# Optimization experiments

Hardware: AMD Instinct MI355X
Metric: run time of the kernel (lower is better)

The kernel has to match this reference:

```python
import jax, jax.numpy as jnp
import numpy as np

N_NODES = 100000
N_EDGES = 3200000
IN_CH = 256
HIDDEN = 64
OUT_CH = 128


def setup_inputs() -> dict:
    key = jax.random.key(0)
    ks = jax.random.split(key, 6)
    x = jax.random.normal(ks[0], (N_NODES, IN_CH), dtype=jnp.float32)
    edge_index = jax.random.randint(ks[1], (2, N_EDGES), 0, N_NODES, dtype=jnp.int64)
    W1 = jax.random.normal(ks[2], (IN_CH, HIDDEN), dtype=jnp.float32) * (1.0 / np.sqrt(IN_CH))
    b1 = jnp.zeros((HIDDEN,), dtype=jnp.float32)
    W2 = jax.random.normal(ks[3], (HIDDEN, OUT_CH), dtype=jnp.float32) * (1.0 / np.sqrt(HIDDEN))
    b2 = jnp.zeros((OUT_CH,), dtype=jnp.float32)
    fcW = jax.random.normal(ks[4], (2, OUT_CH), dtype=jnp.float32) * (1.0 / np.sqrt(OUT_CH))
    fcb = jnp.zeros((2,), dtype=jnp.float32)
    return {"x": x, "edge_index": edge_index, "W1": W1, "b1": b1,
            "W2": W2, "b2": b2, "fcW": fcW, "fcb": fcb}


def _gcn_conv(x, edge_index, W, b):
    """PyG GCNConv: linear transform, add self-loops, symmetric D^-1/2 A D^-1/2 aggregation, bias."""
    N = x.shape[0]
    h = x @ W  # [N, F_out]
    loops = jnp.arange(N, dtype=edge_index.dtype)
    row = jnp.concatenate([edge_index[0], loops])  # source nodes
    col = jnp.concatenate([edge_index[1], loops])  # destination nodes
    deg = jax.ops.segment_sum(jnp.ones_like(col, dtype=h.dtype), col, num_segments=N)
    dinv = jnp.where(deg > 0, jax.lax.rsqrt(deg), 0.0)
    norm = dinv[row] * dinv[col]  # [E+N]
    out = jax.ops.segment_sum(h[row] * norm[:, None], col, num_segments=N)
    return out + b


def reference(x, edge_index, W1, b1, W2, b2, fcW, fcb):
    h = jax.nn.relu(_gcn_conv(x, edge_index, W1, b1))
    h = jax.nn.relu(_gcn_conv(h, edge_index, W2, b2))
    g = jnp.mean(h, axis=0)  # [OUT_CH]
    return g @ fcW.T + fcb   # [2]
```

## Files before the change

kernel.cpp:

```cpp
#include <hip/hip_runtime.h>

#define N_NODES 100000
#define N_EDGES 3200000
#define C_IN 256
#define C_H 64
#define C_OUT 128
#define NB 391
#define BCAP 16384
#define G2F 625
#define NTILES 6250
#define NT16 6250
#define G_GM 1563
#define CH1 8192

typedef unsigned int u32;
typedef unsigned short u16;
typedef unsigned char u8;
typedef unsigned long long u64;
typedef __attribute__((ext_vector_type(8))) short bf16x8;
typedef __attribute__((ext_vector_type(4))) float f32x4;

typedef __attribute__((address_space(3))) unsigned int l_u32;
typedef __attribute__((address_space(1))) const unsigned int g_u32;

__device__ __forceinline__ float bf2f(u16 u) {
    union { u32 i; float f; } v; v.i = ((u32)u) << 16; return v.f;
}
__device__ __forceinline__ u16 f2bf(float f) {
    union { float f; u32 i; } v; v.f = f;
    u32 x = v.i;
    return (u16)((x + 0x7fffu + ((x >> 16) & 1u)) >> 16);
}
__device__ __forceinline__ u8 f2fp8(float f) {
    union { float f; u32 i; } v; v.f = f;
    u32 s = (v.i >> 24) & 0x80u;
    float a = __builtin_fabsf(f);
    a = fminf(a, 448.f);
    if (a < 0.015625f) {
        int m = (int)__builtin_rintf(a * 512.f);
        return (u8)(s | (u32)m);
    }
    union { float ff; u32 i; } w; w.ff = a;
    u32 x = w.i;
    u32 r = x + 0x7FFFFu + ((x >> 20) & 1u);
    u32 E = (r >> 23) - 120u;
    u32 m = (r >> 20) & 7u;
    return (u8)(s | (E << 3) | m);
}

__device__ __forceinline__ void gll16(const void* gp, const void* lp) {
    __builtin_amdgcn_global_load_lds((g_u32*)gp, (l_u32*)lp, 16, 0, 0);
}

#define BT4(a0, a1, a2, a3, r0, r1, r2, r3)                          \
    {                                                                \
        u32 t0 = (a0 & 0x00ff00ffu) | ((a1 & 0x00ff00ffu) << 8);     \
        u32 t1 = ((a0 >> 8) & 0x00ff00ffu) | (a1 & 0xff00ff00u);     \
        u32 t2 = (a2 & 0x00ff00ffu) | ((a3 & 0x00ff00ffu) << 8);     \
        u32 t3 = ((a2 >> 8) & 0x00ff00ffu) | (a3 & 0xff00ff00u);     \
        r0 = (t0 & 0xffffu) | (t2 << 16);                            \
        r2 = (t0 >> 16) | (t2 & 0xffff0000u);                        \
        r1 = (t1 & 0xffffu) | (t3 << 16);                            \
        r3 = (t1 >> 16) | (t3 & 0xffff0000u);                        \
    }

__global__ __launch_bounds__(256) void k_prep(const void* __restrict__ x, const void* __restrict__ ei,
                                              const void* __restrict__ W1, const void* __restrict__ W2,
                                              const void* __restrict__ b1, const void* __restrict__ b2,
                                              const void* __restrict__ fcW, const void* __restrict__ fcb,
                                              int* __restrict__ flags,
                                              u16* __restrict__ W1m, u16* __restrict__ W2m,
                                              u32* __restrict__ bucket_cnt,
                                              float* __restrict__ b1c, float* __restrict__ b2c,
                                              float* __restrict__ fcWc, float* __restrict__ fcbc) {
    __shared__ int sfb;
    int b = blockIdx.x, t = threadIdx.x;
    if (t < 64) {
        u32 wv = ((const u32*)x)[t];
        u32 low = wv & 0xffffu;
        int e = (int)((low >> 7) & 0xff);
        bool inw = (e > 96 && e < 160) || (low == 0);
        u64 m = __ballot(inw);
        if (t == 0) sfb = (__popcll(m) >= 60) ? 1 : 0;
    } else if (b == 0 && t < 128) {
        int i = t - 64;
        u32 wv = ((const u32*)ei)[2 * i + 1];
        u64 m = __ballot(wv == 0);
        if (i == 0) flags[1] = (m == ~0ull) ? 1 : 0;
    }
    __syncthreads();
    int isbf = sfb;
    if (b == 0 && t == 0) flags[0] = isbf;
    int i = b * 256 + t;
    if (i < NB) bucket_cnt[i] = 0;
    if (i < C_IN * C_H) {
        const u16* w1b = (const u16*)W1; const float* w1f = (const float*)W1;
        int j = i & 7, lane = (i >> 3) & 63, nt = (i >> 9) & 3, k0 = i >> 11;
        int k = k0 * 32 + ((lane >> 4) & 3) * 8 + j;
        int n = nt * 16 + (lane & 15);
        W1m[i] = isbf ? w1b[k * C_H + n] : f2bf(w1f[k * C_H + n]);
    } else {
        int i2 = i - C_IN * C_H;
        const u16* w2b = (const u16*)W2; const float* w2f = (const float*)W2;
        int j = i2 & 7, lane = (i2 >> 3) & 63, nt = (i2 >> 9) & 7, k0 = (i2 >> 12) & 1;
        int k = k0 * 32 + ((lane >> 4) & 3) * 8 + j;
        int n = nt * 16 + (lane & 15);
        W2m[i2] = isbf ? w2b[k * C_OUT + n] : f2bf(w2f[k * C_OUT + n]);
    }
    if (b == 0) {
        if (isbf) {
            const u16* p1 = (const u16*)b1;  const u16* p2 = (const u16*)b2;
            const u16* pw = (const u16*)fcW; const u16* pb = (const u16*)fcb;
            for (int q = t; q < C_H; q += 256) b1c[q] = bf2f(p1[q]);
            for (int q = t; q < C_OUT; q += 256) b2c[q] = bf2f(p2[q]);
            for (int q = t; q < 2 * C_OUT; q += 256) fcWc[q] = bf2f(pw[q]);
            for (int q = t; q < 2; q += 256) fcbc[q] = bf2f(pb[q]);
        } else {
            const float* p1 = (const float*)b1;  const float* p2 = (const float*)b2;
            const float* pw = (const float*)fcW; const float* pb = (const float*)fcb;
            for (int q = t; q < C_H; q += 256) b1c[q] = p1[q];
            for (int q = t; q < C_OUT; q += 256) b2c[q] = p2[q];
            for (int q = t; q < 2 * C_OUT; q += 256) fcWc[q] = pw[q];
            for (int q = t; q < 2; q += 256) fcbc[q] = pb[q];
        }
    }
}

__global__ __launch_bounds__(512) void k_scatter1(const int* __restrict__ ei,
                                                  const int* __restrict__ flags,
                                                  u32* __restrict__ bucket_cnt,
                                                  u32* __restrict__ ebuf) {
    __shared__ u32 cnt[NB];
    __shared__ u32 lcur[NB];
    __shared__ u32 gbase[NB];
    __shared__ u32 lofs[512];
    __shared__ u32 stp[CH1];
    __shared__ u16 stb[CH1];
    int t = threadIdx.x;
    int is64 = flags[1];
    int e0 = blockIdx.x * CH1;
    int nv = min(CH1, N_EDGES - e0);
    for (int i = t; i < NB; i += 512) { cnt[i] = 0; lcur[i] = 0; }
    __syncthreads();
    for (int i = t; i < nv; i += 512) {
        int e = e0 + i;
        int d = is64 ? ei[2 * (N_EDGES + e)] : ei[N_EDGES + e];
        atomicAdd(&cnt[d >> 8], 1u);
    }
    __syncthreads();
    u32 v = (t < NB) ? cnt[t] : 0;
    lofs[t] = v;
    __syncthreads();
    for (int off = 1; off < 512; off <<= 1) {
        u32 a = (t >= off) ? lofs[t - off] : 0;
        __syncthreads();
        lofs[t] += a;
        __syncthreads();
    }
    u32 excl = lofs[t] - v;
    __syncthreads();
    lofs[t] = excl;
    __syncthreads();
    for (int i = t; i < nv; i += 512) {
        int e = e0 + i;
        int d, s;
        if (is64) { d = ei[2 * (N_EDGES + e)]; s = ei[2 * e]; }
        else      { d = ei[N_EDGES + e];       s = ei[e]; }
        int b = d >> 8;
        u32 slot = lofs[b] + atomicAdd(&lcur[b], 1u);
        stp[slot] = ((u32)(d & 255) << 20) | (u32)s;
        stb[slot] = (u16)b;
    }
    __syncthreads();
    for (int b = t; b < NB; b += 512) {
        u32 c = cnt[b];
        gbase[b] = c ? atomicAdd(&bucket_cnt[b], c) : 0;
    }
    __syncthreads();
    for (int s = t; s < nv; s += 512) {
        int b = stb[s];
        ebuf[(size_t)b * BCAP + gbase[b] + (s - lofs[b])] = stp[s];
    }
}

__global__ __launch_bounds__(256) void k_scatter2(const u32* __restrict__ bucket_cnt,
                                                  const u32* __restrict__ ebuf,
                                                  int* __restrict__ rowptr,
                                                  float* __restrict__ dinv,
                                                  int* __restrict__ csr) {
    __shared__ u32 ssum[256];
    __shared__ u32 snev;
    __shared__ int cnt[256];
    __shared__ int pfx[256];
    __shared__ int lcur[256];
    int b = blockIdx.x, t = threadIdx.x;
    u32 a = 0;
    for (int i = t; i < NB; i += 256) {
        u32 cv = bucket_cnt[i];
        if (i < b) a += cv;
        if (i == b) snev = cv;
    }
    ssum[t] = a;
    __syncthreads();
    for (int off = 128; off >= 1; off >>= 1) {
        if (t < off) ssum[t] += ssum[t + off];
        __syncthreads();
    }
    int ebeg = (int)ssum[0];
    int ne = (int)snev;
    const u32* src = ebuf + (size_t)b * BCAP;
    int sbeg = ebeg + (b << 8);
    cnt[t] = 0;
    lcur[t] = 0;
    __syncthreads();
    for (int i = t; i < ne; i += 256)
        atomicAdd(&cnt[(src[i] >> 20) & 255], 1);
    __syncthreads();
    int v = cnt[t];
    pfx[t] = v;
    __syncthreads();
    for (int off = 1; off < 256; off <<= 1) {
        int pv = (t >= off) ? pfx[t - off] : 0;
        __syncthreads();
        pfx[t] += pv;
        __syncthreads();
    }
    int node = (b << 8) + t;
    int rstart = sbeg + (pfx[t] - v) + t;
    if (node < N_NODES) {
        rowptr[node] = rstart;
        dinv[node] = rsqrtf((float)(v + 1));
        csr[rstart] = node << 6;
        if (node == N_NODES - 1) {
            rowptr[N_NODES] = rstart + v + 1;
            for (int i = 0; i < 64; ++i) csr[rstart + v + 1 + i] = 0;
        }
    }
    __syncthreads();
    for (int i = t; i < ne; i += 256) {
        u32 p = src[i];
        int dl = (p >> 20) & 255;
        int pos = sbeg + (pfx[dl] - cnt[dl]) + dl + 1 + atomicAdd(&lcur[dl], 1);
        csr[pos] = (int)((p & 0x1FFFFu) << 6);
    }
}

__global__ __launch_bounds__(256) void k_gemm1(const void* __restrict__ xv,
                                               const u16* __restrict__ W1m,
                                               const float* __restrict__ dinv,
                                               u8* __restrict__ g1,
                                               const int* __restrict__ flags) {
    __shared__ u16 wlds[C_IN * C_H];
    int t = threadIdx.x;
    int isbf = flags[0];
    {
        const uint4* src = (const uint4*)W1m;
        uint4* dst = (uint4*)wlds;
#pragma unroll
        for (int it = 0; it < 8; ++it) dst[t + it * 256] = src[t + it * 256];
    }
    __syncthreads();
    int w = t >> 6, lane = t & 63;
    int quad = lane >> 4, mrow = lane & 15;
    int m0 = blockIdx.x * 128 + w * 32;
    if (m0 >= N_NODES) return;

    bf16x8 a[2][8];
    if (isbf) {
        const u16* xb = (const u16*)xv;
#pragma unroll
        for (int mt = 0; mt < 2; ++mt)
#pragma unroll
            for (int k0 = 0; k0 < 8; ++k0)
                a[mt][k0] = *(const bf16x8*)(xb + (size_t)(m0 + mt * 16 + mrow) * C_IN + k0 * 32 + quad * 8);
    } else {
        const float* xf = (const float*)xv;
#pragma unroll
        for (int mt = 0; mt < 2; ++mt)
#pragma unroll
            for (int k0 = 0; k0 < 8; ++k0) {
                const float* p = xf + (size_t)(m0 + mt * 16 + mrow) * C_IN + k0 * 32 + quad * 8;
                float4 v0 = *(const float4*)p;
                float4 v1 = *(const float4*)(p + 4);
                bf16x8 r;
                r[0] = (short)f2bf(v0.x); r[1] = (short)f2bf(v0.y);
                r[2] = (short)f2bf(v0.z); r[3] = (short)f2bf(v0.w);
                r[4] = (short)f2bf(v1.x); r[5] = (short)f2bf(v1.y);
                r[6] = (short)f2bf(v1.z); r[7] = (short)f2bf(v1.w);
                a[mt][k0] = r;
            }
    }

    float dv0[4], dv1[4];
#pragma unroll
    for (int r = 0; r < 4; ++r) {
        dv0[r] = dinv[m0 + quad * 4 + r] * 16.f;
        dv1[r] = dinv[m0 + 16 + quad * 4 + r] * 16.f;
    }

#pragma unroll
    for (int nt = 0; nt < 4; ++nt) {
        bf16x8 b[8];
#pragma unroll
        for (int k0 = 0; k0 < 8; ++k0)
            b[k0] = *(const bf16x8*)&wlds[((k0 * 4 + nt) * 64 + lane) * 8];
        f32x4 acc0 = {0.f, 0.f, 0.f, 0.f};
        f32x4 acc1 = {0.f, 0.f, 0.f, 0.f};
#pragma unroll
        for (int k0 = 0; k0 < 8; ++k0) {
            acc0 = __builtin_amdgcn_mfma_f32_16x16x32_bf16(a[0][k0], b[k0], acc0, 0, 0, 0);
            acc1 = __builtin_amdgcn_mfma_f32_16x16x32_bf16(a[1][k0], b[k0], acc1, 0, 0, 0);
        }
        int pos = mrow * 4 + nt;
#pragma unroll
        for (int r = 0; r < 4; ++r) {
            g1[(size_t)(m0 + quad * 4 + r) * C_H + pos] = f2fp8(acc0[r] * dv0[r]);
            g1[(size_t)(m0 + 16 + quad * 4 + r) * C_H + pos] = f2fp8(acc1[r] * dv1[r]);
        }
    }
}

template <int MODE>
__global__ __launch_bounds__(256) void k_gatherM(const int* __restrict__ rowptr,
                                                 const int* __restrict__ csrb,
                                                 const float* __restrict__ dinv,
                                                 const u8* __restrict__ gt,
                                                 const float* __restrict__ bias,
                                                 void* __restrict__ out) {
    __shared__ __align__(16) u8 hsb[4][4096];
    __shared__ u64 lut8[81];
    int t = threadIdx.x;
    if (t < 81) {
        int s = t / 9, e = t - s * 9;
        u32 lo = 0, hi = 0;
#pragma unroll
        for (int j = 0; j < 4; ++j) if (j >= s && j < e) lo |= 0x18u << (8 * j);
#pragma unroll
        for (int j = 4; j < 8; ++j) if (j >= s && j < e) hi |= 0x18u << (8 * (j - 4));
        lut8[t] = ((u64)hi << 32) | lo;
    }
    __syncthreads();
    int w = t >> 6, lane = t & 63;
    int tile = blockIdx.x * 4 + w;
    if (tile >= NT16) return;

    int cg = lane >> 4, c = lane & 15;
    int n0 = tile << 4;
    int lo = rowptr[n0 + c];
    int hi = rowptr[n0 + c + 1];
    int beg = __shfl(lo, 0, 64);
    int end = __shfl(hi, 15, 64);
    int rowA = ((lane >> 2) & 3) * 8 + (lane >> 4);
    int rowB = rowA + 4;
    int s16 = (lane & 3) * 16;
    const char* gb = (const char*)gt;
    u8* hw = hsb[w];
    int bi = cg * 16 + c;
    f32x4 acc0 = {0.f, 0.f, 0.f, 0.f}, acc1 = acc0, acc2 = acc0, acc3 = acc0;
    int nch = (end - beg + 31) >> 5;
    int cb = beg;
    {
        u32 oA = (u32)csrb[cb + rowA];
        u32 oB = (u32)csrb[cb + rowB];
        gll16(gb + oA + s16, hw);
        gll16(gb + oB + s16, hw + 1024);
        asm volatile("" ::: "memory");
    }
    for (int ci = 0; ci < nch; ++ci) {
        int cbn = cb + 32;
        bool more = (ci + 1 < nch);
        u32 nA = 0, nB = 0;
        if (more) {
            nA = (u32)csrb[cbn + rowA];
            nB = (u32)csrb[cbn + rowB];
        }
        if (more) asm volatile("s_waitcnt vmcnt(2)" ::: "memory");
        else      asm volatile("s_waitcnt vmcnt(0)" ::: "memory");
        const u32* hb = (const u32*)(hw + ((ci & 1) << 11));
        u32 w0 = hb[bi], w1 = hb[bi + 64], w2 = hb[bi + 128], w3 = hb[bi + 192];
        u32 w4 = hb[bi + 256], w5 = hb[bi + 320], w6 = hb[bi + 384], w7 = hb[bi + 448];
        u32 l0, l1, l2, l3, h0, h1, h2, h3;
        BT4(w0, w1, w2, w3, l0, l1, l2, l3)
        BT4(w4, w5, w6, w7, h0, h1, h2, h3)
        int cbg = cb + cg * 8;
        int s0 = min(max(lo - cbg, 0), 8);
        int e0 = min(max(hi - cbg, 0), 8);
        union P8 { u32 u[2]; long l; } pa, pb0, pb1, pb2, pb3;
        u64 av = lut8[s0 * 9 + e0];
        pa.u[0] = (u32)av; pa.u[1] = (u32)(av >> 32);
        pb0.u[0] = l0; pb0.u[1] = h0;
        pb1.u[0] = l1; pb1.u[1] = h1;
        pb2.u[0] = l2; pb2.u[1] = h2;
        pb3.u[0] = l3; pb3.u[1] = h3;
        acc0 = __builtin_amdgcn_mfma_f32_16x16x32_fp8_fp8(pa.l, pb0.l, acc0, 0, 0, 0);
        acc1 = __builtin_amdgcn_mfma_f32_16x16x32_fp8_fp8(pa.l, pb1.l, acc1, 0, 0, 0);
        acc2 = __builtin_amdgcn_mfma_f32_16x16x32_fp8_fp8(pa.l, pb2.l, acc2, 0, 0, 0);
        acc3 = __builtin_amdgcn_mfma_f32_16x16x32_fp8_fp8(pa.l, pb3.l, acc3, 0, 0, 0);
        if (more) {
            int bo = ((ci + 1) & 1) << 11;
            gll16(gb + nA + s16, hw + bo);
            gll16(gb + nB + s16, hw + bo + 1024);
            asm volatile("" ::: "memory");
        }
        cb = cbn;
    }
    float dv[4];
    int nb = n0 + cg * 4;
#pragma unroll
    for (int q = 0; q < 4; ++q) dv[q] = dinv[nb + q];
    if (MODE == 0) {
        u8* ob = (u8*)out + (size_t)nb * C_H + c * 4;
#define EPI(ACC, CHT)                                                                       \
        {                                                                                   \
            float bs = bias[CHT * 16 + c];                                                  \
            _Pragma("unroll")                                                               \
            for (int q = 0; q < 4; ++q)                                                     \
                ob[q * C_H + CHT] =                                                         \
                    f2fp8(16.f * dv[q] * fmaxf(dv[q] * ACC[q] + bs, 0.f));                  \
        }
        EPI(acc0, 0) EPI(acc1, 1) EPI(acc2, 2) EPI(acc3, 3)
#undef EPI
    } else {
        u16* ob = (u16*)out + (size_t)nb * C_H + c;
#define EPI(ACC, CHT)                                                                       \
        {                                                                                   \
            _Pragma("unroll")                                                               \
            for (int q = 0; q < 4; ++q)                                                     \
                ob[q * C_H + CHT * 16] = f2bf(dv[q] * ACC[q]);                              \
        }
        EPI(acc0, 0) EPI(acc1, 1) EPI(acc2, 2) EPI(acc3, 3)
#undef EPI
    }
}

__global__ __launch_bounds__(256) void k_fused2(const u16* __restrict__ aggb,
                                                const u16* __restrict__ W2m,
                                                const float* __restrict__ b2c,
                                                float* __restrict__ partial) {
    __shared__ float psum[4 * 8 * 64];
    int t = threadIdx.x;
    int w = t >> 6, lane = t & 63;
    int quad = lane >> 4, m = lane & 15;

    bf16x8 b[2][8];
#pragma unroll
    for (int k0 = 0; k0 < 2; ++k0)
#pragma unroll
        for (int nt = 0; nt < 8; ++nt)
            b[k0][nt] = *(const bf16x8*)&W2m[((k0 * 8 + nt) * 64 + lane) * 8];

    float pacc[8] = {0.f, 0.f, 0.f, 0.f, 0.f, 0.f, 0.f, 0.f};
    float bias[8];
#pragma unroll
    for (int nt = 0; nt < 8; ++nt) bias[nt] = b2c[nt * 16 + m];

    for (int tile = blockIdx.x * 4 + w; tile < NTILES; tile += G2F * 4) {
        const u16* arow = aggb + (size_t)(tile * 16 + m) * C_H + quad * 8;
        bf16x8 a0 = *(const bf16x8*)(arow);
        bf16x8 a1 = *(const bf16x8*)(arow + 32);
#pragma unroll
        for (int nt = 0; nt < 8; ++nt) {
            f32x4 acc = {0.f, 0.f, 0.f, 0.f};
            acc = __builtin_amdgcn_mfma_f32_16x16x32_bf16(a0, b[0][nt], acc, 0, 0, 0);
            acc = __builtin_amdgcn_mfma_f32_16x16x32_bf16(a1, b[1][nt], acc, 0, 0, 0);
#pragma unroll
            for (int r = 0; r < 4; ++r)
                pacc[nt] += fmaxf(acc[r] + bias[nt], 0.f);
        }
    }
#pragma unroll
    for (int nt = 0; nt < 8; ++nt) psum[(w * 8 + nt) * 64 + lane] = pacc[nt];
    __syncthreads();
    if (t < 128) {
        int nt = t >> 4, m2 = t & 15;
        float s = 0.f;
#pragma unroll
        for (int ww = 0; ww < 4; ++ww)
#pragma unroll
            for (int q = 0; q < 4; ++q)
                s += psum[(ww * 8 + nt) * 64 + q * 16 + m2];
        partial[blockIdx.x * C_OUT + t] = s;
    }
}

__global__ __launch_bounds__(512) void k_final(const float* __restrict__ partial,
                                               const float* __restrict__ fcWc,
                                               const float* __restrict__ fcbc,
                                               void* __restrict__ out,
                                               const int* __restrict__ flags) {
    __shared__ float sm[512];
    __shared__ float red[256];
    int t = threadIdx.x;
    int f = t & 127, c = t >> 7;
    float s = 0.f;
    for (int b = c; b < G2F; b += 4) s += partial[b * 128 + f];
    sm[t] = s;
    __syncthreads();
    if (t < 128) {
        float gm = (sm[t] + sm[t + 128] + sm[t + 256] + sm[t + 384]) * (1.0f / (float)N_NODES);
        red[t] = gm * fcWc[t];
        red[128 + t] = gm * fcWc[128 + t];
    }
    __syncthreads();
    for (int off = 64; off >= 1; off >>= 1) {
        if (t < off) {
            red[t] += red[t + off];
            red[128 + t] += red[128 + t + off];
        }
        __syncthreads();
    }
    if (t == 0) {
        float o0 = red[0] + fcbc[0];
        float o1 = red[128] + fcbc[1];
        if (flags[0]) {
            u16* ob = (u16*)out;
            ob[0] = f2bf(o0);
            ob[1] = f2bf(o1);
        } else {
            float* of = (float*)out;
            of[0] = o0;
            of[1] = o1;
        }
    }
}

#define OFF_FLAGS   0u
#define OFF_DINV    512u
#define OFF_ROWPTR  400896u
#define OFF_BCNT    801280u
#define OFF_CSR     1201664u
#define OFF_H1      14402560u
#define OFF_A1      27202560u
#define OFF_AGG     40002560u
#define OFF_PART    52802560u
#define OFF_W1C     53122560u
#define OFF_W2C     53155328u
#define OFF_B1C     53171712u
#define OFF_B2C     53171968u
#define OFF_FCWC    53172480u
#define OFF_FCBC    53173504u
#define OFF_EBUF    53174272u

extern "C" void kernel_launch(void* const* d_in, const int* in_sizes, int n_in,
                              void* d_out, int out_size, void* d_ws, size_t ws_size,
                              hipStream_t stream) {
    (void)in_sizes; (void)n_in; (void)out_size; (void)ws_size;
    const void* x   = d_in[0];
    const int*  ei  = (const int*)d_in[1];
    const void* W1  = d_in[2];
    const void* b1  = d_in[3];
    const void* W2  = d_in[4];
    const void* b2  = d_in[5];
    const void* fcW = d_in[6];
    const void* fcb = d_in[7];

    char* ws = (char*)d_ws;
    int*   flags  = (int*)(ws + OFF_FLAGS);
    float* dinv   = (float*)(ws + OFF_DINV);
    int*   rowptr = (int*)(ws + OFF_ROWPTR);
    u32*   bcnt   = (u32*)(ws + OFF_BCNT);
    int*   csr    = (int*)(ws + OFF_CSR);
    u8*    g1     = (u8*)(ws + OFF_H1);
    u8*    a1s    = (u8*)(ws + OFF_A1);
    u16*   aggb   = (u16*)(ws + OFF_AGG);
    u32*   ebuf   = (u32*)(ws + OFF_EBUF);
    float* partial= (float*)(ws + OFF_PART);
    u16*   W1m    = (u16*)(ws + OFF_W1C);
    u16*   W2m    = (u16*)(ws + OFF_W2C);
    float* b1c    = (float*)(ws + OFF_B1C);
    float* b2c    = (float*)(ws + OFF_B2C);
    float* fcWc   = (float*)(ws + OFF_FCWC);
    float* fcbc   = (float*)(ws + OFF_FCBC);

    k_prep<<<96, 256, 0, stream>>>(x, ei, W1, W2, b1, b2, fcW, fcb,
                                   flags, W1m, W2m, bcnt, b1c, b2c, fcWc, fcbc);
    k_scatter1<<<NB, 512, 0, stream>>>(ei, flags, bcnt, ebuf);
    k_scatter2<<<NB, 256, 0, stream>>>(bcnt, ebuf, rowptr, dinv, csr);
    k_gemm1<<<(N_NODES + 127) / 128, 256, 0, stream>>>(x, W1m, dinv, g1, flags);
    k_gatherM<0><<<G_GM, 256, 0, stream>>>(rowptr, csr, dinv, g1, b1c, (void*)a1s);
    k_gatherM<1><<<G_GM, 256, 0, stream>>>(rowptr, csr, dinv, a1s, b2c, (void*)aggb);
    k_fused2<<<G2F, 256, 0, stream>>>(aggb, W2m, b2c, partial);
    k_final<<<1, 512, 0, stream>>>(partial, fcWc, fcbc, (void*)d_out, flags);
}
```

Baseline: 357.7 us.

## Deepen gather pipeline to four LDS buffers with two-chunk prefetch

The neighbor-gather kernel's edge loop now uses four LDS buffers per wave instead of two. Index loads run three chunks ahead and the async global-to-LDS row gathers run two chunks ahead. Waitcnt thresholds are adjusted to match, and the loop is unrolled by two so the register sets holding prefetched offsets alternate. The goal is to hide more of the random-gather memory latency, at the cost of doubling LDS per block, which may lower occupancy.

Result: no change. 361.4 us (+1.0%).

```diff
diff --git a/kernel.cpp b/kernel.cpp
--- a/kernel.cpp
+++ b/kernel.cpp
@@ -327,7 +327,7 @@
                                                  const u8* __restrict__ gt,
                                                  const float* __restrict__ bias,
                                                  void* __restrict__ out) {
-    __shared__ __align__(16) u8 hsb[4][4096];
+    __shared__ __align__(16) u8 hsb[4][8192];
     __shared__ u64 lut8[81];
     int t = threadIdx.x;
     if (t < 81) {
@@ -359,51 +359,100 @@
     f32x4 acc0 = {0.f, 0.f, 0.f, 0.f}, acc1 = acc0, acc2 = acc0, acc3 = acc0;
     int nch = (end - beg + 31) >> 5;
     int cb = beg;
-    {
-        u32 oA = (u32)csrb[cb + rowA];
-        u32 oB = (u32)csrb[cb + rowB];
-        gll16(gb + oA + s16, hw);
-        gll16(gb + oB + s16, hw + 1024);
-        asm volatile("" ::: "memory");
-    }
-    for (int ci = 0; ci < nch; ++ci) {
-        int cbn = cb + 32;
-        bool more = (ci + 1 < nch);
-        u32 nA = 0, nB = 0;
-        if (more) {
-            nA = (u32)csrb[cbn + rowA];
-            nB = (u32)csrb[cbn + rowB];
-        }
-        if (more) asm volatile("s_waitcnt vmcnt(2)" ::: "memory");
-        else      asm volatile("s_waitcnt vmcnt(0)" ::: "memory");
-        const u32* hb = (const u32*)(hw + ((ci & 1) << 11));
-        u32 w0 = hb[bi], w1 = hb[bi + 64], w2 = hb[bi + 128], w3 = hb[bi + 192];
-        u32 w4 = hb[bi + 256], w5 = hb[bi + 320], w6 = hb[bi + 384], w7 = hb[bi + 448];
-        u32 l0, l1, l2, l3, h0, h1, h2, h3;
-        BT4(w0, w1, w2, w3, l0, l1, l2, l3)
-        BT4(w4, w5, w6, w7, h0, h1, h2, h3)
-        int cbg = cb + cg * 8;
-        int s0 = min(max(lo - cbg, 0), 8);
-        int e0 = min(max(hi - cbg, 0), 8);
-        union P8 { u32 u[2]; long l; } pa, pb0, pb1, pb2, pb3;
-        u64 av = lut8[s0 * 9 + e0];
-        pa.u[0] = (u32)av; pa.u[1] = (u32)(av >> 32);
-        pb0.u[0] = l0; pb0.u[1] = h0;
-        pb1.u[0] = l1; pb1.u[1] = h1;
-        pb2.u[0] = l2; pb2.u[1] = h2;
-        pb3.u[0] = l3; pb3.u[1] = h3;
-        acc0 = __builtin_amdgcn_mfma_f32_16x16x32_fp8_fp8(pa.l, pb0.l, acc0, 0, 0, 0);
-        acc1 = __builtin_amdgcn_mfma_f32_16x16x32_fp8_fp8(pa.l, pb1.l, acc1, 0, 0, 0);
-        acc2 = __builtin_amdgcn_mfma_f32_16x16x32_fp8_fp8(pa.l, pb2.l, acc2, 0, 0, 0);
-        acc3 = __builtin_amdgcn_mfma_f32_16x16x32_fp8_fp8(pa.l, pb3.l, acc3, 0, 0, 0);
-        if (more) {
-            int bo = ((ci + 1) & 1) << 11;
-            gll16(gb + nA + s16, hw + bo);
-            gll16(gb + nB + s16, hw + bo + 1024);
-            asm volatile("" ::: "memory");
-        }
-        cb = cbn;
-    }
+
+#define GCHUNK(BO)                                                                 \
+    {                                                                              \
+        const u32* hb = (const u32*)(hw + (BO));                                   \
+        u32 w0 = hb[bi], w1 = hb[bi + 64], w2 = hb[bi + 128], w3 = hb[bi + 192];   \
+        u32 w4 = hb[bi + 256], w5 = hb[bi + 320], w6 = hb[bi + 384],               \
+            w7 = hb[bi + 448];                                                     \
+        u32 l0, l1, l2, l3, h0, h1, h2, h3;                                        \
+        BT4(w0, w1, w2, w3, l0, l1, l2, l3)                                        \
+        BT4(w4, w5, w6, w7, h0, h1, h2, h3)                                        \
+        int cbg = cb + cg * 8;                                                     \
+        int s0 = min(max(lo - cbg, 0), 8);                                         \
+        int e0v = min(max(hi - cbg, 0), 8);                                        \
+        union P8 { u32 u[2]; long l; } pa, pb0, pb1, pb2, pb3;                     \
+        u64 av = lut8[s0 * 9 + e0v];                                               \
+        pa.u[0] = (u32)av; pa.u[1] = (u32)(av >> 32);                              \
+        pb0.u[0] = l0; pb0.u[1] = h0;                                              \
+        pb1.u[0] = l1; pb1.u[1] = h1;                                              \
+        pb2.u[0] = l2; pb2.u[1] = h2;                                              \
+        pb3.u[0] = l3; pb3.u[1] = h3;                                              \
+        acc0 = __builtin_amdgcn_mfma_f32_16x16x32_fp8_fp8(pa.l, pb0.l, acc0, 0, 0, 0); \
+        acc1 = __builtin_amdgcn_mfma_f32_16x16x32_fp8_fp8(pa.l, pb1.l, acc1, 0, 0, 0); \
+        acc2 = __builtin_amdgcn_mfma_f32_16x16x32_fp8_fp8(pa.l, pb2.l, acc2, 0, 0, 0); \
+        acc3 = __builtin_amdgcn_mfma_f32_16x16x32_fp8_fp8(pa.l, pb3.l, acc3, 0, 0, 0); \
+    }
+#define WAITK(M1, M2)                                                  \
+    if (M2)      asm volatile("s_waitcnt vmcnt(4)" ::: "memory");      \
+    else if (M1) asm volatile("s_waitcnt vmcnt(2)" ::: "memory");      \
+    else         asm volatile("s_waitcnt vmcnt(0)" ::: "memory");
+#define PIN asm volatile("" ::: "memory");
+
+    u32 eA = (u32)csrb[cb + rowA], eB = (u32)csrb[cb + rowB];
+    PIN
+    gll16(gb + eA + s16, hw);
+    gll16(gb + eB + s16, hw + 1024);
+    PIN
+    u32 oA = 0, oB = 0;
+    if (nch > 1) {
+        oA = (u32)csrb[cb + 32 + rowA];
+        oB = (u32)csrb[cb + 32 + rowB];
+        PIN
+        gll16(gb + oA + s16, hw + 2048);
+        gll16(gb + oB + s16, hw + 3072);
+    }
+    PIN
+    if (nch > 2) {
+        eA = (u32)csrb[cb + 64 + rowA];
+        eB = (u32)csrb[cb + 64 + rowB];
+    }
+    PIN
+    int ci = 0;
+    while (true) {
+        {
+            bool m1 = ci + 1 < nch, m2 = ci + 2 < nch, m3 = ci + 3 < nch;
+            WAITK(m1, m2)
+            GCHUNK((ci & 3) << 11)
+            PIN
+            if (m3) {
+                oA = (u32)csrb[cb + 96 + rowA];
+                oB = (u32)csrb[cb + 96 + rowB];
+            }
+            PIN
+            if (m2) {
+                int bo = ((ci + 2) & 3) << 11;
+                gll16(gb + eA + s16, hw + bo);
+                gll16(gb + eB + s16, hw + bo + 1024);
+            }
+            PIN
+            ++ci; cb += 32;
+            if (ci >= nch) break;
+        }
+        {
+            bool m1 = ci + 1 < nch, m2 = ci + 2 < nch, m3 = ci + 3 < nch;
+            WAITK(m1, m2)
+            GCHUNK((ci & 3) << 11)
+            PIN
+            if (m3) {
+                eA = (u32)csrb[cb + 96 + rowA];
+                eB = (u32)csrb[cb + 96 + rowB];
+            }
+            PIN
+            if (m2) {
+                int bo = ((ci + 2) & 3) << 11;
+                gll16(gb + oA + s16, hw + bo);
+                gll16(gb + oB + s16, hw + bo + 1024);
+            }
+            PIN
+            ++ci; cb += 32;
+            if (ci >= nch) break;
+        }
+    }
+#undef GCHUNK
+#undef WAITK
+#undef PIN
     float dv[4];
     int nb = n0 + cg * 4;
 #pragma unroll
```

## Fuse layer-2 GEMM and mean pooling into gather epilogue; cache edges in scatter1

Applied to the files above, without the earlier changes.

The second gather kernel now stages its aggregated bf16 tile in LDS and runs the W2 MFMA, bias, ReLU and per-block column sum in its epilogue. This removes the bf16 aggregate round trip through global memory and the separate k_fused2 launch. The final reduction now sums over G_GM partial blocks instead of G2F. Separately, k_scatter1 keeps the 16 edge endpoints each thread reads in registers, so edge_index is read from global memory once rather than twice. The tradeoffs are higher register pressure and per-tile W2 loads from global/L2, plus a larger partial buffer to reduce.

After: 404.5 us. 13.1% more time.

```diff
diff --git a/kernel.cpp b/kernel.cpp
--- a/kernel.cpp
+++ b/kernel.cpp
@@ -7,7 +7,6 @@
 #define C_OUT 128
 #define NB 391
 #define BCAP 16384
-#define G2F 625
 #define NTILES 6250
 #define NT16 6250
 #define G_GM 1563
@@ -142,10 +141,18 @@
     int nv = min(CH1, N_EDGES - e0);
     for (int i = t; i < NB; i += 512) { cnt[i] = 0; lcur[i] = 0; }
     __syncthreads();
-    for (int i = t; i < nv; i += 512) {
-        int e = e0 + i;
-        int d = is64 ? ei[2 * (N_EDGES + e)] : ei[N_EDGES + e];
-        atomicAdd(&cnt[d >> 8], 1u);
+    u32 dr[16], sr[16];
+#pragma unroll
+    for (int it = 0; it < 16; ++it) {
+        int i = t + it * 512;
+        if (i < nv) {
+            int e = e0 + i;
+            int d, s;
+            if (is64) { d = ei[2 * (N_EDGES + e)]; s = ei[2 * e]; }
+            else      { d = ei[N_EDGES + e];       s = ei[e]; }
+            dr[it] = (u32)d; sr[it] = (u32)s;
+            atomicAdd(&cnt[d >> 8], 1u);
+        }
     }
     __syncthreads();
     u32 v = (t < NB) ? cnt[t] : 0;
@@ -161,15 +168,16 @@
     __syncthreads();
     lofs[t] = excl;
     __syncthreads();
-    for (int i = t; i < nv; i += 512) {
-        int e = e0 + i;
-        int d, s;
-        if (is64) { d = ei[2 * (N_EDGES + e)]; s = ei[2 * e]; }
-        else      { d = ei[N_EDGES + e];       s = ei[e]; }
-        int b = d >> 8;
-        u32 slot = lofs[b] + atomicAdd(&lcur[b], 1u);
-        stp[slot] = ((u32)(d & 255) << 20) | (u32)s;
-        stb[slot] = (u16)b;
+#pragma unroll
+    for (int it = 0; it < 16; ++it) {
+        int i = t + it * 512;
+        if (i < nv) {
+            int d = (int)dr[it], s = (int)sr[it];
+            int b = d >> 8;
+            u32 slot = lofs[b] + atomicAdd(&lcur[b], 1u);
+            stp[slot] = ((u32)(d & 255) << 20) | (u32)s;
+            stb[slot] = (u16)b;
+        }
     }
     __syncthreads();
     for (int b = t; b < NB; b += 512) {
@@ -326,6 +334,7 @@
                                                  const float* __restrict__ dinv,
                                                  const u8* __restrict__ gt,
                                                  const float* __restrict__ bias,
+                                                 const u16* __restrict__ W2m,
                                                  void* __restrict__ out) {
     __shared__ __align__(16) u8 hsb[4][4096];
     __shared__ u64 lut8[81];
@@ -342,73 +351,78 @@
     __syncthreads();
     int w = t >> 6, lane = t & 63;
     int tile = blockIdx.x * 4 + w;
-    if (tile >= NT16) return;
+    bool active = tile < NT16;
 
     int cg = lane >> 4, c = lane & 15;
     int n0 = tile << 4;
-    int lo = rowptr[n0 + c];
-    int hi = rowptr[n0 + c + 1];
-    int beg = __shfl(lo, 0, 64);
-    int end = __shfl(hi, 15, 64);
-    int rowA = ((lane >> 2) & 3) * 8 + (lane >> 4);
-    int rowB = rowA + 4;
-    int s16 = (lane & 3) * 16;
-    const char* gb = (const char*)gt;
     u8* hw = hsb[w];
-    int bi = cg * 16 + c;
     f32x4 acc0 = {0.f, 0.f, 0.f, 0.f}, acc1 = acc0, acc2 = acc0, acc3 = acc0;
-    int nch = (end - beg + 31) >> 5;
-    int cb = beg;
-    {
-        u32 oA = (u32)csrb[cb + rowA];
-        u32 oB = (u32)csrb[cb + rowB];
-        gll16(gb + oA + s16, hw);
-        gll16(gb + oB + s16, hw + 1024);
-        asm volatile("" ::: "memory");
-    }
-    for (int ci = 0; ci < nch; ++ci) {
-        int cbn = cb + 32;
-        bool more = (ci + 1 < nch);
-        u32 nA = 0, nB = 0;
-        if (more) {
-            nA = (u32)csrb[cbn + rowA];
-            nB = (u32)csrb[cbn + rowB];
-        }
-        if (more) asm volatile("s_waitcnt vmcnt(2)" ::: "memory");
-        else      asm volatile("s_waitcnt vmcnt(0)" ::: "memory");
-        const u32* hb = (const u32*)(hw + ((ci & 1) << 11));
-        u32 w0 = hb[bi], w1 = hb[bi + 64], w2 = hb[bi + 128], w3 = hb[bi + 192];
-        u32 w4 = hb[bi + 256], w5 = hb[bi + 320], w6 = hb[bi + 384], w7 = hb[bi + 448];
-        u32 l0, l1, l2, l3, h0, h1, h2, h3;
-        BT4(w0, w1, w2, w3, l0, l1, l2, l3)
-        BT4(w4, w5, w6, w7, h0, h1, h2, h3)
-        int cbg = cb + cg * 8;
-        int s0 = min(max(lo - cbg, 0), 8);
-        int e0 = min(max(hi - cbg, 0), 8);
-        union P8 { u32 u[2]; long l; } pa, pb0, pb1, pb2, pb3;
-        u64 av = lut8[s0 * 9 + e0];
-        pa.u[0] = (u32)av; pa.u[1] = (u32)(av >> 32);
-        pb0.u[0] = l0; pb0.u[1] = h0;
-        pb1.u[0] = l1; pb1.u[1] = h1;
-        pb2.u[0] = l2; pb2.u[1] = h2;
-        pb3.u[0] = l3; pb3.u[1] = h3;
-        acc0 = __builtin_amdgcn_mfma_f32_16x16x32_fp8_fp8(pa.l, pb0.l, acc0, 0, 0, 0);
-        acc1 = __builtin_amdgcn_mfma_f32_16x16x32_fp8_fp8(pa.l, pb1.l, acc1, 0, 0, 0);
-        acc2 = __builtin_amdgcn_mfma_f32_16x16x32_fp8_fp8(pa.l, pb2.l, acc2, 0, 0, 0);
-        acc3 = __builtin_amdgcn_mfma_f32_16x16x32_fp8_fp8(pa.l, pb3.l, acc3, 0, 0, 0);
-        if (more) {
-            int bo = ((ci + 1) & 1) << 11;
-            gll16(gb + nA + s16, hw + bo);
-            gll16(gb + nB + s16, hw + bo + 1024);
+    int lo = 0, hi = 0;
+    if (active) {
+        lo = rowptr[n0 + c];
+        hi = rowptr[n0 + c + 1];
+        int beg = __shfl(lo, 0, 64);
+        int end = __shfl(hi, 15, 64);
+        int rowA = ((lane >> 2) & 3) * 8 + (lane >> 4);
+        int rowB = rowA + 4;
+        int s16 = (lane & 3) * 16;
+        const char* gb = (const char*)gt;
+        int bi = cg * 16 + c;
+        int nch = (end - beg + 31) >> 5;
+        int cb = beg;
+        {
+            u32 oA = (u32)csrb[cb + rowA];
+            u32 oB = (u32)csrb[cb + rowB];
+            gll16(gb + oA + s16, hw);
+            gll16(gb + oB + s16, hw + 1024);
             asm volatile("" ::: "memory");
         }
-        cb = cbn;
-    }
-    float dv[4];
-    int nb = n0 + cg * 4;
-#pragma unroll
-    for (int q = 0; q < 4; ++q) dv[q] = dinv[nb + q];
-    if (MODE == 0) {
+        for (int ci = 0; ci < nch; ++ci) {
+            int cbn = cb + 32;
+            bool more = (ci + 1 < nch);
+            u32 nA = 0, nB = 0;
+            if (more) {
+                nA = (u32)csrb[cbn + rowA];
+                nB = (u32)csrb[cbn + rowB];
+            }
+            if (more) asm volatile("s_waitcnt vmcnt(2)" ::: "memory");
+            else      asm volatile("s_waitcnt vmcnt(0)" ::: "memory");
+            const u32* hb = (const u32*)(hw + ((ci & 1) << 11));
+            u32 w0 = hb[bi], w1 = hb[bi + 64], w2 = hb[bi + 128], w3 = hb[bi + 192];
+            u32 w4 = hb[bi + 256], w5 = hb[bi + 320], w6 = hb[bi + 384], w7 = hb[bi + 448];
+            u32 l0, l1, l2, l3, h0, h1, h2, h3;
+            BT4(w0, w1, w2, w3, l0, l1, l2, l3)
+            BT4(w4, w5, w6, w7, h0, h1, h2, h3)
+            int cbg = cb + cg * 8;
+            int s0 = min(max(lo - cbg, 0), 8);
+            int e0v = min(max(hi - cbg, 0), 8);
+            union P8 { u32 u[2]; long l; } pa, pb0, pb1, pb2, pb3;
+            u64 av = lut8[s0 * 9 + e0v];
+            pa.u[0] = (u32)av; pa.u[1] = (u32)(av >> 32);
+            pb0.u[0] = l0; pb0.u[1] = h0;
+            pb1.u[0] = l1; pb1.u[1] = h1;
+            pb2.u[0] = l2; pb2.u[1] = h2;
+            pb3.u[0] = l3; pb3.u[1] = h3;
+            acc0 = __builtin_amdgcn_mfma_f32_16x16x32_fp8_fp8(pa.l, pb0.l, acc0, 0, 0, 0);
+            acc1 = __builtin_amdgcn_mfma_f32_16x16x32_fp8_fp8(pa.l, pb1.l, acc1, 0, 0, 0);
+            acc2 = __builtin_amdgcn_mfma_f32_16x16x32_fp8_fp8(pa.l, pb2.l, acc2, 0, 0, 0);
+            acc3 = __builtin_amdgcn_mfma_f32_16x16x32_fp8_fp8(pa.l, pb3.l, acc3, 0, 0, 0);
+            if (more) {
+                int bo = ((ci + 1) & 1) << 11;
+                gll16(gb + nA + s16, hw + bo);
+                gll16(gb + nB + s16, hw + bo + 1024);
+                asm volatile("" ::: "memory");
+            }
+            cb = cbn;
+        }
+    }
+
+    if constexpr (MODE == 0) {
+        if (!active) return;
+        float dv[4];
+        int nb = n0 + cg * 4;
+#pragma unroll
+        for (int q = 0; q < 4; ++q) dv[q] = dinv[nb + q];
         u8* ob = (u8*)out + (size_t)nb * C_H + c * 4;
 #define EPI(ACC, CHT)                                                                       \
         {                                                                                   \
@@ -421,65 +435,55 @@
         EPI(acc0, 0) EPI(acc1, 1) EPI(acc2, 2) EPI(acc3, 3)
 #undef EPI
     } else {
-        u16* ob = (u16*)out + (size_t)nb * C_H + c;
-#define EPI(ACC, CHT)                                                                       \
-        {                                                                                   \
-            _Pragma("unroll")                                                               \
-            for (int q = 0; q < 4; ++q)                                                     \
-                ob[q * C_H + CHT * 16] = f2bf(dv[q] * ACC[q]);                              \
-        }
-        EPI(acc0, 0) EPI(acc1, 1) EPI(acc2, 2) EPI(acc3, 3)
-#undef EPI
-    }
-}
-
-__global__ __launch_bounds__(256) void k_fused2(const u16* __restrict__ aggb,
-                                                const u16* __restrict__ W2m,
-                                                const float* __restrict__ b2c,
-                                                float* __restrict__ partial) {
-    __shared__ float psum[4 * 8 * 64];
-    int t = threadIdx.x;
-    int w = t >> 6, lane = t & 63;
-    int quad = lane >> 4, m = lane & 15;
-
-    bf16x8 b[2][8];
-#pragma unroll
-    for (int k0 = 0; k0 < 2; ++k0)
-#pragma unroll
-        for (int nt = 0; nt < 8; ++nt)
-            b[k0][nt] = *(const bf16x8*)&W2m[((k0 * 8 + nt) * 64 + lane) * 8];
-
-    float pacc[8] = {0.f, 0.f, 0.f, 0.f, 0.f, 0.f, 0.f, 0.f};
-    float bias[8];
-#pragma unroll
-    for (int nt = 0; nt < 8; ++nt) bias[nt] = b2c[nt * 16 + m];
-
-    for (int tile = blockIdx.x * 4 + w; tile < NTILES; tile += G2F * 4) {
-        const u16* arow = aggb + (size_t)(tile * 16 + m) * C_H + quad * 8;
-        bf16x8 a0 = *(const bf16x8*)(arow);
-        bf16x8 a1 = *(const bf16x8*)(arow + 32);
-#pragma unroll
-        for (int nt = 0; nt < 8; ++nt) {
-            f32x4 acc = {0.f, 0.f, 0.f, 0.f};
-            acc = __builtin_amdgcn_mfma_f32_16x16x32_bf16(a0, b[0][nt], acc, 0, 0, 0);
-            acc = __builtin_amdgcn_mfma_f32_16x16x32_bf16(a1, b[1][nt], acc, 0, 0, 0);
-#pragma unroll
-            for (int r = 0; r < 4; ++r)
-                pacc[nt] += fmaxf(acc[r] + bias[nt], 0.f);
-        }
-    }
-#pragma unroll
-    for (int nt = 0; nt < 8; ++nt) psum[(w * 8 + nt) * 64 + lane] = pacc[nt];
-    __syncthreads();
-    if (t < 128) {
-        int nt = t >> 4, m2 = t & 15;
-        float s = 0.f;
-#pragma unroll
-        for (int ww = 0; ww < 4; ++ww)
-#pragma unroll
-            for (int q = 0; q < 4; ++q)
-                s += psum[(ww * 8 + nt) * 64 + q * 16 + m2];
-        partial[blockIdx.x * C_OUT + t] = s;
+        float pacc[8] = {0.f, 0.f, 0.f, 0.f, 0.f, 0.f, 0.f, 0.f};
+        if (active) {
+            float dv[4];
+            int nb = n0 + cg * 4;
+#pragma unroll
+            for (int q = 0; q < 4; ++q) dv[q] = dinv[nb + q];
+            u16* a2 = (u16*)hw;
+#define ST(ACC, CHT)                                                                        \
+            {                                                                               \
+                _Pragma("unroll")                                                           \
+                for (int q = 0; q < 4; ++q)                                                 \
+                    a2[(cg * 4 + q) * 72 + CHT * 16 + c] = f2bf(dv[q] * ACC[q]);            \
+            }
+            ST(acc0, 0) ST(acc1, 1) ST(acc2, 2) ST(acc3, 3)
+#undef ST
+            asm volatile("s_waitcnt lgkmcnt(0)" ::: "memory");
+            __builtin_amdgcn_sched_barrier(0);
+            bf16x8 af0 = *(const bf16x8*)&a2[c * 72 + cg * 8];
+            bf16x8 af1 = *(const bf16x8*)&a2[c * 72 + 32 + cg * 8];
+            asm volatile("s_waitcnt lgkmcnt(0)" ::: "memory");
+            __builtin_amdgcn_sched_barrier(0);
+#pragma unroll
+            for (int nt = 0; nt < 8; ++nt) {
+                bf16x8 b0 = *(const bf16x8*)&W2m[((0 * 8 + nt) * 64 + lane) * 8];
+                bf16x8 b1 = *(const bf16x8*)&W2m[((1 * 8 + nt) * 64 + lane) * 8];
+                f32x4 av = {0.f, 0.f, 0.f, 0.f};
+                av = __builtin_amdgcn_mfma_f32_16x16x32_bf16(af0, b0, av, 0, 0, 0);
+                av = __builtin_amdgcn_mfma_f32_16x16x32_bf16(af1, b1, av, 0, 0, 0);
+                float bs = bias[nt * 16 + c];
+#pragma unroll
+                for (int r = 0; r < 4; ++r)
+                    pacc[nt] += fmaxf(av[r] + bs, 0.f);
+            }
+        }
+        __syncthreads();
+        float* psum = (float*)&hsb[0][0];
+#pragma unroll
+        for (int nt = 0; nt < 8; ++nt) psum[(w * 8 + nt) * 64 + lane] = pacc[nt];
+        __syncthreads();
+        if (t < 128) {
+            int nt = t >> 4, m2 = t & 15;
+            float s = 0.f;
+#pragma unroll
+            for (int ww = 0; ww < 4; ++ww)
+#pragma unroll
+                for (int q = 0; q < 4; ++q)
+                    s += psum[(ww * 8 + nt) * 64 + q * 16 + m2];
+            ((float*)out)[blockIdx.x * C_OUT + t] = s;
+        }
     }
 }
 
@@ -493,7 +497,7 @@
     int t = threadIdx.x;
     int f = t & 127, c = t >> 7;
     float s = 0.f;
-    for (int b = c; b < G2F; b += 4) s += partial[b * 128 + f];
+    for (int b = c; b < G_GM; b += 4) s += partial[b * 128 + f];
     sm[t] = s;
     __syncthreads();
     if (t < 128) {
@@ -531,8 +535,7 @@
 #define OFF_CSR     1201664u
 #define OFF_H1      14402560u
 #define OFF_A1      27202560u
-#define OFF_AGG     40002560u
-#define OFF_PART    52802560u
+#define OFF_PART    40002560u
 #define OFF_W1C     53122560u
 #define OFF_W2C     53155328u
 #define OFF_B1C     53171712u
@@ -562,7 +565,6 @@
     int*   csr    = (int*)(ws + OFF_CSR);
     u8*    g1     = (u8*)(ws + OFF_H1);
     u8*    a1s    = (u8*)(ws + OFF_A1);
-    u16*   aggb   = (u16*)(ws + OFF_AGG);
     u32*   ebuf   = (u32*)(ws + OFF_EBUF);
     float* partial= (float*)(ws + OFF_PART);
     u16*   W1m    = (u16*)(ws + OFF_W1C);
@@ -577,8 +579,7 @@
     k_scatter1<<<NB, 512, 0, stream>>>(ei, flags, bcnt, ebuf);
     k_scatter2<<<NB, 256, 0, stream>>>(bcnt, ebuf, rowptr, dinv, csr);
     k_gemm1<<<(N_NODES + 127) / 128, 256, 0, stream>>>(x, W1m, dinv, g1, flags);
-    k_gatherM<0><<<G_GM, 256, 0, stream>>>(rowptr, csr, dinv, g1, b1c, (void*)a1s);
-    k_gatherM<1><<<G_GM, 256, 0, stream>>>(rowptr, csr, dinv, a1s, b2c, (void*)aggb);
-    k_fused2<<<G2F, 256, 0, stream>>>(aggb, W2m, b2c, partial);
+    k_gatherM<0><<<G_GM, 256, 0, stream>>>(rowptr, csr, dinv, g1, b1c, W2m, (void*)a1s);
+    k_gatherM<1><<<G_GM, 256, 0, stream>>>(rowptr, csr, dinv, a1s, b2c, W2m, (void*)partial);
     k_final<<<1, 512, 0, stream>>>(partial, fcWc, fcbc, (void*)d_out, flags);
 }
```
